# Kernel tuning notes

Hardware: AMD Instinct MI355X
Metric: run time of the kernel (lower is better)

The kernel has to match this reference:

```python
import jax, jax.numpy as jnp
import numpy as np
from jax import lax

B, DIM, H, W = 4, 256, 32, 32
NH = 8
HD = DIM // NH            # 32; CDA uses doubled head dim 2*HD=64
HIDDEN = 512              # FFN hidden, multiple of DIM (groups=DIM dwconv)
DEPTH = 1
LAMBDA_INIT = 0.8 - 0.6 * float(np.exp(-0.3 * DEPTH))
EPS = 1e-5


def conv1x1(w, x):
    # w: (out,in), x: (b,in,h,w)
    return jnp.einsum('oi,bihw->bohw', w, x)


def dwconv(x, w, groups):
    return lax.conv_general_dilated(x, w, (1, 1), 'SAME',
                                    dimension_numbers=('NCHW', 'OIHW', 'NCHW'),
                                    feature_group_count=groups)


def layernorm_c(x, wgt, bias):
    # WithBias LayerNorm over channel dim (to_3d -> LN(-1) -> to_4d)
    mu = jnp.mean(x, axis=1, keepdims=True)
    var = jnp.mean((x - mu) ** 2, axis=1, keepdims=True)
    return (x - mu) / jnp.sqrt(var + EPS) * wgt[None, :, None, None] + bias[None, :, None, None]


def batchnorm(x, g, b, m, v):
    return (x - m[None, :, None, None]) / jnp.sqrt(v[None, :, None, None] + EPS) \
        * g[None, :, None, None] + b[None, :, None, None]


def _cda(x, wq, wk, wv, lq1, lk1, lq2, lk2, rms_scale, wo):
    b, c, hh, ww = x.shape
    n = hh * ww

    def heads(wp):
        t = conv1x1(wp, x).reshape(b, NH, 2 * HD, n)
        return jnp.transpose(t, (0, 1, 3, 2))  # b h n (2hd)

    Q, K, V = heads(wq), heads(wk), heads(wv)
    scale = HD ** -0.5
    a1 = jax.nn.softmax(jnp.einsum('bhnd,bhmd->bhnm', Q[..., :HD], K[..., :HD]) * scale, axis=-1)
    a2 = jax.nn.softmax(jnp.einsum('bhnd,bhmd->bhnm', Q[..., HD:], K[..., HD:]) * scale, axis=-1)
    lam = jnp.exp(jnp.sum(lq1 * lk1, -1)) - jnp.exp(jnp.sum(lq2 * lk2, -1)) + LAMBDA_INIT  # (NH,)
    out = jnp.einsum('bhnm,bhmd->bhnd', a1 - lam[None, :, None, None] * a2, V)
    rms = jnp.sqrt(jnp.mean(out * out, axis=-1, keepdims=True) + EPS)
    out = out / rms * rms_scale * (1.0 - LAMBDA_INIT)
    out = jnp.transpose(out, (0, 1, 3, 2)).reshape(b, 2 * c, hh, ww)
    return conv1x1(wo, out)


def _cha(x, temp, wqkv, wdw, wout):
    b, c, hh, ww = x.shape
    n = hh * ww
    qkv = dwconv(conv1x1(wqkv, x), wdw, 3 * DIM)
    r = qkv.reshape(b, 3, NH, c // NH, n)
    q, k, v = r[:, 0], r[:, 1], r[:, 2]
    q = q / jnp.maximum(jnp.linalg.norm(q, axis=-1, keepdims=True), 1e-12)
    k = k / jnp.maximum(jnp.linalg.norm(k, axis=-1, keepdims=True), 1e-12)
    attn = jax.nn.softmax(jnp.einsum('bhcn,bhdn->bhcd', q, k) * temp[None, :, None, None], axis=-1)
    out = jnp.einsum('bhcd,bhdn->bhcn', attn, v).reshape(b, c, hh, ww)
    return conv1x1(wout, out)


def _ffn(x, bn1_g, bn1_b, bn1_m, bn1_v, w1, b1, bn2_g, bn2_b, bn2_m, bn2_v, w2, b2, w3, b3):
    h = batchnorm(x, bn1_g, bn1_b, bn1_m, bn1_v)
    h = conv1x1(w1, h) + b1[None, :, None, None]
    h = batchnorm(h, bn2_g, bn2_b, bn2_m, bn2_v)
    h = dwconv(h, w2, DIM) + b2[None, :, None, None]
    h = jnp.clip(h, 0.0, 6.0)  # ReLU6
    return conv1x1(w3, h) + b3[None, :, None, None]


def setup_inputs() -> dict:
    key = jax.random.key(0)
    ks = jax.random.split(key, 20)
    nrm = lambda i, shape, s=0.02: jax.random.normal(ks[i], shape, jnp.float32) * s
    return {
        'x': jax.random.normal(ks[0], (B, DIM, H, W), jnp.float32),
        'ln1_w': jnp.ones((DIM,), jnp.float32), 'ln1_b': jnp.zeros((DIM,), jnp.float32),
        'cda_wq': nrm(1, (2 * DIM, DIM)), 'cda_wk': nrm(2, (2 * DIM, DIM)), 'cda_wv': nrm(3, (2 * DIM, DIM)),
        'cda_lq1': nrm(4, (NH, HD), 0.1), 'cda_lk1': nrm(5, (NH, HD), 0.1),
        'cda_lq2': nrm(6, (NH, HD), 0.1), 'cda_lk2': nrm(7, (NH, HD), 0.1),
        'cda_rms_scale': jnp.ones((2 * HD,), jnp.float32), 'cda_wo': nrm(8, (DIM, 2 * DIM)),
        'ln2_w': jnp.ones((DIM,), jnp.float32), 'ln2_b': jnp.zeros((DIM,), jnp.float32),
        'cha_temp': jnp.ones((NH,), jnp.float32),
        'cha_wqkv': nrm(9, (3 * DIM, DIM)), 'cha_wdw': nrm(10, (3 * DIM, 1, 3, 3), 0.1),
        'cha_wout': nrm(11, (DIM, DIM)),
        'ln3_w': jnp.ones((DIM,), jnp.float32), 'ln3_b': jnp.zeros((DIM,), jnp.float32),
        'bn1_g': jnp.ones((DIM,), jnp.float32), 'bn1_b': jnp.zeros((DIM,), jnp.float32),
        'bn1_m': nrm(12, (DIM,), 0.1), 'bn1_v': jnp.ones((DIM,), jnp.float32),
        'ffn_w1': nrm(13, (HIDDEN, DIM)), 'ffn_b1': jnp.zeros((HIDDEN,), jnp.float32),
        'bn2_g': jnp.ones((HIDDEN,), jnp.float32), 'bn2_b': jnp.zeros((HIDDEN,), jnp.float32),
        'bn2_m': nrm(14, (HIDDEN,), 0.1), 'bn2_v': jnp.ones((HIDDEN,), jnp.float32),
        'ffn_w2': nrm(15, (HIDDEN, HIDDEN // DIM, 3, 3), 0.1), 'ffn_b2': jnp.zeros((HIDDEN,), jnp.float32),
        'ffn_w3': nrm(16, (DIM, HIDDEN)), 'ffn_b3': jnp.zeros((DIM,), jnp.float32),
    }


def reference(x, ln1_w, ln1_b, cda_wq, cda_wk, cda_wv, cda_lq1, cda_lk1, cda_lq2, cda_lk2,
              cda_rms_scale, cda_wo, ln2_w, ln2_b, cha_temp, cha_wqkv, cha_wdw, cha_wout,
              ln3_w, ln3_b, bn1_g, bn1_b, bn1_m, bn1_v, ffn_w1, ffn_b1, bn2_g, bn2_b,
              bn2_m, bn2_v, ffn_w2, ffn_b2, ffn_w3, ffn_b3):
    h = layernorm_c(x, ln1_w, ln1_b)
    x = x + _cda(h, cda_wq, cda_wk, cda_wv, cda_lq1, cda_lk1, cda_lq2, cda_lk2, cda_rms_scale, cda_wo)
    h = layernorm_c(x, ln2_w, ln2_b)
    x = x + _cha(h, cha_temp, cha_wqkv, cha_wdw, cha_wout)
    h = layernorm_c(x, ln3_w, ln3_b)
    x = x + _ffn(h, bn1_g, bn1_b, bn1_m, bn1_v, ffn_w1, ffn_b1, bn2_g, bn2_b, bn2_m, bn2_v, ffn_w2, ffn_b2, ffn_w3, ffn_b3)
    return x
```

## Files before the change

kernel.cpp:

```cpp
#include <hip/hip_runtime.h>
#include <hip/hip_bf16.h>

typedef __hip_bfloat16 bf16;
typedef __attribute__((ext_vector_type(8))) short s16x8;
typedef __attribute__((ext_vector_type(4))) float f32x4;

#define DEV __device__ __forceinline__

DEV float b2f(bf16 v){ return __bfloat162float(v); }
DEV ushort f2bf(float f){ bf16 h = __float2bfloat16(f); return *reinterpret_cast<ushort*>(&h); }

constexpr int NPIX = 1024;
constexpr float EPSF = 1e-5f;
constexpr float LAMBDA_INIT_F = 0.3555090675909693f;
constexpr float ONE_M_LI     = 0.6444909324090307f;
constexpr float ATT_SCALE    = 0.17677669529663687f;

constexpr size_t OFF_WBF   = 2120448;
constexpr size_t OFF_QT    = 2644736;
constexpr size_t OFF_V16   = 4741888;
constexpr size_t OFF_ATT   = 5790464;
constexpr size_t OFF_BUF1  = 6839040;
constexpr size_t OFF_BUF2  = 9984768;
constexpr size_t OFF_SPART = 13130496;
constexpr size_t OFF_STATS = 13425408;
constexpr size_t OFF_EFF   = 13449984;
constexpr size_t OFF_FLAG  = 13452608;

struct PackArgs { const void* p[34]; };

__global__ __launch_bounds__(256) void detect_kernel(const void* __restrict__ x, int* __restrict__ flag){
  __shared__ int sh;
  if (threadIdx.x == 0) sh = 0;
  __syncthreads();
  const bf16* h = (const bf16*)x;
  int local = 0;
  for (int i = threadIdx.x; i < 4096; i += 256){
    float v = b2f(h[i]);
    if (!(fabsf(v) <= 1e6f)) local = 1;
  }
  if (local) atomicOr(&sh, 1);
  __syncthreads();
  if (threadIdx.x == 0) *flag = sh;
}

DEV float rdin(const PackArgs& a, int i, int idx, int flag){
  return flag ? ((const float*)a.p[i])[idx] : b2f(((const bf16*)a.p[i])[idx]);
}

__global__ __launch_bounds__(256) void prep_all_kernel(PackArgs args, const int* __restrict__ flagp,
    float* __restrict__ P, ushort* __restrict__ W, float* __restrict__ eff, float* __restrict__ stats){
  __shared__ float ps[16][64], ps2[16][64];
  const int t = threadIdx.x;
  const int blk = blockIdx.x;
  const int flag = *flagp;
  if (blk < 8283){
    constexpr int NIN = 34;
    constexpr int off[NIN+1] = {0,1048576,1048832,1049088,1180160,1311232,1442304,1442560,
      1442816,1443072,1443328,1443392,1574464,1574720,1574976,1574984,1771592,1778504,
      1844040,1844296,1844552,1844808,1845064,1845320,1845576,1976648,1977160,1977672,
      1978184,1978696,1979208,1988424,1988936,2120008,2120264};
    const int g = blk*256 + t;
    if (g >= off[NIN]) return;
    int idx = 0;
    #pragma unroll
    for (int k = 1; k < NIN; k++) idx = (g >= off[k]) ? k : idx;
    P[g] = rdin(args, idx, g - off[idx], flag);
  } else if (blk < 9307){
    const int g = (blk - 8283)*1024 + t*4;
    int src, loc;
    if      (g <  131072){ src = 3;  loc = g; }
    else if (g <  262144){ src = 4;  loc = g - 131072; }
    else if (g <  393216){ src = 5;  loc = g - 262144; }
    else if (g <  589824){ src = 15; loc = g - 393216; }
    else if (g <  720896){ src = 11; loc = g - 589824; }
    else if (g <  786432){ src = 17; loc = g - 720896; }
    else if (g <  917504){ src = 24; loc = g - 786432; }
    else                 { src = 32; loc = g - 917504; }
    ushort4 o;
    if (flag){
      const float4 v = *(const float4*)((const float*)args.p[src] + loc);
      o = make_ushort4(f2bf(v.x), f2bf(v.y), f2bf(v.z), f2bf(v.w));
    } else {
      o = *(const ushort4*)((const ushort*)args.p[src] + loc);
    }
    *(ushort4*)&W[g] = o;
  } else if (blk == 9307){
    eff[t]      = rdin(args,1,t,flag);  eff[256+t] = rdin(args,2,t,flag);
    eff[512+t]  = rdin(args,12,t,flag); eff[768+t] = rdin(args,13,t,flag);
    const float s1 = rdin(args,20,t,flag) * rsqrtf(rdin(args,23,t,flag) + EPSF);
    eff[1024+t] = rdin(args,18,t,flag) * s1;
    eff[1280+t] = (rdin(args,19,t,flag) - rdin(args,22,t,flag)) * s1 + rdin(args,21,t,flag);
    for (int c = t; c < 512; c += 256){
      const float sc = rdin(args,26,c,flag) * rsqrtf(rdin(args,29,c,flag) + EPSF);
      eff[1536+c] = sc;
      eff[2048+c] = rdin(args,27,c,flag) - rdin(args,28,c,flag)*sc;
    }
    if (t < 8){
      float e1 = 0.f, e2 = 0.f;
      for (int i = 0; i < 32; i++){
        e1 += rdin(args,6,t*32+i,flag) * rdin(args,7,t*32+i,flag);
        e2 += rdin(args,8,t*32+i,flag) * rdin(args,9,t*32+i,flag);
      }
      eff[2560+t] = __expf(e1) - __expf(e2) + LAMBDA_INIT_F;
    }
    for (int i = t; i < 16384; i += 256) stats[8192 + i] = 0.f;
  } else {
    const int bi = blk - 9308;
    const int b = bi >> 4, n0 = (bi & 15)*64;
    const int tn = t & 15, tc = t >> 4;
    float s = 0.f, q = 0.f;
    #pragma unroll 4
    for (int i = 0; i < 16; i++){
      const int c = tc*16 + i;
      #pragma unroll
      for (int j = 0; j < 4; j++){
        const float v = rdin(args, 0, ((b*256 + c) << 10) + n0 + tn*4 + j, flag);
        s += v; q += v*v;
      }
    }
    ps[tc][tn*4+0] = 0.f;
    ps[tc][tn*4] = 0.f;
    float sj[4] = {0,0,0,0}, qj[4] = {0,0,0,0};
    #pragma unroll 4
    for (int i = 0; i < 16; i++){
      const int c = tc*16 + i;
      #pragma unroll
      for (int j = 0; j < 4; j++){
        const float v = rdin(args, 0, ((b*256 + c) << 10) + n0 + tn*4 + j, flag);
        sj[j] += v; qj[j] += v*v;
      }
    }
    #pragma unroll
    for (int j = 0; j < 4; j++){ ps[tc][tn*4+j] = sj[j]; ps2[tc][tn*4+j] = qj[j]; }
    __syncthreads();
    if (t < 64){
      float a = 0.f, qq = 0.f;
      #pragma unroll
      for (int j2 = 0; j2 < 16; j2++){ a += ps[j2][t]; qq += ps2[j2][t]; }
      stats[(size_t)b*NPIX + n0 + t] = a;
      stats[4096 + (size_t)b*NPIX + n0 + t] = qq;
    }
  }
}

template<int INM, int EPIM, bool BIAS, bool BN2F, bool STATS>
__global__ __launch_bounds__(256) void gemm_kernel(
    const float* __restrict__ Xf, const ushort* __restrict__ Xb, const ushort* __restrict__ W,
    const float* __restrict__ bias, const float* __restrict__ mu, const float* __restrict__ rstd,
    const float* __restrict__ effw, const float* __restrict__ effb,
    const float* __restrict__ s2, const float* __restrict__ t2,
    const float* __restrict__ res, void* __restrict__ out,
    ushort* __restrict__ qt, ushort* __restrict__ v16,
    float* __restrict__ gstats,
    int Cin, const int* __restrict__ flag)
{
  __shared__ ushort Xt[64][72];
  const int t = threadIdx.x;
  const int nb = blockIdx.x*64, ob = blockIdx.y*64, b = blockIdx.z;
  const int lane = t & 63, w = t >> 6;
  const int wR = w >> 1, wC = w & 1;
  const int l15 = lane & 15, g = lane >> 4;
  const int tn = t & 63, tc4 = t >> 6;
  const f32x4 z4 = {0.f,0.f,0.f,0.f};
  f32x4 acc[2][2] = {{z4,z4},{z4,z4}};

  for (int kb = 0; kb < Cin; kb += 64){
    if (INM == 2){
      const ushort* src = Xb + ((size_t)b*NPIX + nb + tn)*Cin + kb + tc4*16;
      *(uint4*)&Xt[tn][tc4*16]   = *(const uint4*)src;
      *(uint4*)&Xt[tn][tc4*16+8] = *(const uint4*)(src+8);
    } else {
      float m_ = 0.f, r_ = 1.f;
      if (INM == 0){
        const float sv = mu[(size_t)b*NPIX + nb + tn];
        const float qv = rstd[(size_t)b*NPIX + nb + tn];
        m_ = sv * (1.f/256.f);
        const float var = qv*(1.f/256.f) - m_*m_;
        r_ = rsqrtf(fmaxf(var, 0.f) + EPSF);
      }
      ushort tmp[16];
      #pragma unroll
      for (int i = 0; i < 16; i++){
        const int c = kb + tc4*16 + i;
        float v = Xf[((size_t)b*Cin + c)*NPIX + nb + tn];
        if (INM == 0) v = (v - m_)*r_*effw[c] + effb[c];
        tmp[i] = f2bf(v);
      }
      *(uint4*)&Xt[tn][tc4*16]   = *(uint4*)&tmp[0];
      *(uint4*)&Xt[tn][tc4*16+8] = *(uint4*)&tmp[8];
    }
    __syncthreads();
    #pragma unroll
    for (int ks = 0; ks < 2; ks++){
      const s16x8 a0 = *(const s16x8*)&W[(size_t)(ob + wR*32 + l15)*Cin + kb + ks*32 + g*8];
      const s16x8 a1 = *(const s16x8*)&W[(size_t)(ob + wR*32 + 16 + l15)*Cin + kb + ks*32 + g*8];
      const s16x8 b0 = *(const s16x8*)&Xt[wC*32 + l15][ks*32 + g*8];
      const s16x8 b1 = *(const s16x8*)&Xt[wC*32 + 16 + l15][ks*32 + g*8];
      acc[0][0] = __builtin_amdgcn_mfma_f32_16x16x32_bf16(a0, b0, acc[0][0], 0,0,0);
      acc[0][1] = __builtin_amdgcn_mfma_f32_16x16x32_bf16(a0, b1, acc[0][1], 0,0,0);
      acc[1][0] = __builtin_amdgcn_mfma_f32_16x16x32_bf16(a1, b0, acc[1][0], 0,0,0);
      acc[1][1] = __builtin_amdgcn_mfma_f32_16x16x32_bf16(a1, b1, acc[1][1], 0,0,0);
    }
    __syncthreads();
  }

  const int Cout = gridDim.y*64;
  float sst[2] = {0.f, 0.f}, qst[2] = {0.f, 0.f};
  #pragma unroll
  for (int fr = 0; fr < 2; fr++){
    #pragma unroll
    for (int fc = 0; fc < 2; fc++){
      const int o = ob + wR*32 + fr*16 + 4*g;
      const int n = nb + wC*32 + fc*16 + l15;
      const f32x4 v = acc[fr][fc];
      if (EPIM == 0){
        if (ob < 1024){
          const int qk = o >> 9, h = (o >> 6) & 7, d = o & 63;
          ushort4 pk = make_ushort4(f2bf(v[0]), f2bf(v[1]), f2bf(v[2]), f2bf(v[3]));
          ushort* dst = qt + ((((size_t)qk*4 + b)*8 + h)*NPIX + n)*64 + d;
          *(ushort4*)dst = pk;
        } else {
          const int c = o - 1024;
          #pragma unroll
          for (int r = 0; r < 4; r++)
            v16[((size_t)b*512 + c + r)*NPIX + n] = f2bf(v[r]);
        }
      } else {
        #pragma unroll
        for (int r = 0; r < 4; r++){
          float val = v[r];
          if (BIAS) val += bias[o + r];
          if (BN2F) val = val*s2[o+r] + t2[o+r];
          const size_t row = ((size_t)b*Cout + o + r)*NPIX + n;
          if (EPIM == 1){
            const float vf = val + res[row];
            ((float*)out)[row] = vf;
            if (STATS){ sst[fc] += vf; qst[fc] += vf*vf; }
          }
          else if (EPIM == 2){ ((float*)out)[row] = val; }
          else {
            val += res[row];
            if (*flag) ((float*)out)[row] = val;
            else       ((ushort*)out)[row] = f2bf(val);
          }
        }
      }
    }
  }
  if (STATS){
    float* sacc = (float*)&Xt[0][0];
    if (t < 128) sacc[t] = 0.f;
    __syncthreads();
    #pragma unroll
    for (int fc = 0; fc < 2; fc++){
      const int nl = wC*32 + fc*16 + l15;
      atomicAdd(&sacc[nl*2+0], sst[fc]);
      atomicAdd(&sacc[nl*2+1], qst[fc]);
    }
    __syncthreads();
    if (t < 64){
      atomicAdd(&gstats[(size_t)b*NPIX + nb + t],        sacc[t*2+0]);
      atomicAdd(&gstats[4096 + (size_t)b*NPIX + nb + t], sacc[t*2+1]);
    }
  }
}

__global__ __launch_bounds__(256) void attn_kernel(
    const ushort* __restrict__ QT, const ushort* __restrict__ V16,
    const float* __restrict__ Pf, const float* __restrict__ lamArr,
    ushort* __restrict__ att)
{
  __shared__ ushort Ks[2][4096];
  __shared__ ushort Vs[2][4096];
  const int t = threadIdx.x;
  const int lane = t & 63, w = t >> 6;
  const int l15 = lane & 15, g = lane >> 4;
  const int qt = blockIdx.x, h = blockIdx.y, b = blockIdx.z;
  const int qsub = qt*64 + w*16;
  const ushort* Qb = QT + ((size_t)b*8 + h)*NPIX*64;
  const ushort* Kb = QT + ((size_t)(4 + b)*8 + h)*NPIX*64;
  const ushort* Vb = V16 + ((size_t)b*512 + h*64)*NPIX;

  const int c0row = t >> 3, c0col = t & 7;
  const int c1row = (t + 256) >> 3, c1col = t & 7;
  const int sw0 = (c0col ^ (c0row & 7))*8;
  const int sw1 = (c1col ^ (c1row & 7))*8;

  s16x8 bq[2];
  #pragma unroll
  for (int hx = 0; hx < 2; hx++)
    bq[hx] = *(const s16x8*)&Qb[(size_t)(qsub + l15)*64 + 32*hx + 8*g];
  const float lam = lamArr[h];

  const f32x4 z4 = {0.f,0.f,0.f,0.f};
  f32x4 o0[4] = {z4,z4,z4,z4};
  f32x4 o1[4] = {z4,z4,z4,z4};
  float z[2] = {0.f, 0.f};

  uint4 kra = *(const uint4*)&Kb[(size_t)c0row*64 + c0col*8];
  uint4 krb = *(const uint4*)&Kb[(size_t)c1row*64 + c1col*8];
  uint4 vra = *(const uint4*)&Vb[(size_t)c0row*NPIX + c0col*8];
  uint4 vrb = *(const uint4*)&Vb[(size_t)c1row*NPIX + c1col*8];
  *(uint4*)&Ks[0][c0row*64 + sw0] = kra;
  *(uint4*)&Ks[0][c1row*64 + sw1] = krb;
  *(uint4*)&Vs[0][c0row*64 + sw0] = vra;
  *(uint4*)&Vs[0][c1row*64 + sw1] = vrb;
  kra = *(const uint4*)&Kb[(size_t)(64 + c0row)*64 + c0col*8];
  krb = *(const uint4*)&Kb[(size_t)(64 + c1row)*64 + c1col*8];
  vra = *(const uint4*)&Vb[(size_t)c0row*NPIX + 64 + c0col*8];
  vrb = *(const uint4*)&Vb[(size_t)c1row*NPIX + 64 + c1col*8];
  __syncthreads();

  #pragma unroll 1
  for (int it = 0; it < 16; it++){
    const int cur = it & 1;
    const ushort* Kc = &Ks[cur][0];
    const ushort* Vc = &Vs[cur][0];

    f32x4 s[2][4];
    #pragma unroll
    for (int fr = 0; fr < 4; fr++){
      const int row = fr*16 + l15;
      const int rx = (row & 7)*8;
      #pragma unroll
      for (int hx = 0; hx < 2; hx++){
        const s16x8 ak = *(const s16x8*)&Kc[row*64 + ((hx*32 + 8*g) ^ rx)];
        s[hx][fr] = __builtin_amdgcn_mfma_f32_16x16x32_bf16(ak, bq[hx], z4, 0,0,0);
      }
    }
    s16x8 pa[2][2];
    #pragma unroll
    for (int hx = 0; hx < 2; hx++){
      #pragma unroll
      for (int ms = 0; ms < 2; ms++){
        ushort tmp[8];
        #pragma unroll
        for (int fr2 = 0; fr2 < 2; fr2++)
          #pragma unroll
          for (int r = 0; r < 4; r++){
            const float e = __expf(s[hx][ms*2 + fr2][r] * ATT_SCALE);
            z[hx] += e;
            tmp[fr2*4 + r] = f2bf(e);
          }
        pa[hx][ms] = *(s16x8*)tmp;
      }
    }
    __builtin_amdgcn_s_setprio(1);
    #pragma unroll
    for (int ms = 0; ms < 2; ms++){
      #pragma unroll
      for (int dc = 0; dc < 4; dc++){
        const int row = dc*16 + l15;
        const int r7 = row & 7;
        const int elo = ms*32 + 4*g;
        const int eloswz = ((((elo >> 3) ^ r7) << 3) | (elo & 7));
        const int ehi = elo + 16;
        const int ehiswz = ((((ehi >> 3) ^ r7) << 3) | (ehi & 7));
        const uint2 lo = *(const uint2*)&Vc[row*64 + eloswz];
        const uint2 hi = *(const uint2*)&Vc[row*64 + ehiswz];
        union { uint u[4]; s16x8 v; } bv;
        bv.u[0] = lo.x; bv.u[1] = lo.y; bv.u[2] = hi.x; bv.u[3] = hi.y;
        o0[dc] = __builtin_amdgcn_mfma_f32_16x16x32_bf16(pa[0][ms], bv.v, o0[dc], 0,0,0);
        o1[dc] = __builtin_amdgcn_mfma_f32_16x16x32_bf16(pa[1][ms], bv.v, o1[dc], 0,0,0);
      }
    }
    __builtin_amdgcn_s_setprio(0);

    if (it < 15){
      const int nxt = cur ^ 1;
      *(uint4*)&Ks[nxt][c0row*64 + sw0] = kra;
      *(uint4*)&Ks[nxt][c1row*64 + sw1] = krb;
      *(uint4*)&Vs[nxt][c0row*64 + sw0] = vra;
      *(uint4*)&Vs[nxt][c1row*64 + sw1] = vrb;
      if (it < 14){
        const int m0 = (it + 2)*64;
        kra = *(const uint4*)&Kb[(size_t)(m0 + c0row)*64 + c0col*8];
        krb = *(const uint4*)&Kb[(size_t)(m0 + c1row)*64 + c1col*8];
        vra = *(const uint4*)&Vb[(size_t)c0row*NPIX + m0 + c0col*8];
        vrb = *(const uint4*)&Vb[(size_t)c1row*NPIX + m0 + c1col*8];
      }
    }
    __syncthreads();
  }

  #pragma unroll
  for (int hx = 0; hx < 2; hx++){
    z[hx] += __shfl_xor(z[hx], 16);
    z[hx] += __shfl_xor(z[hx], 32);
  }
  float zi0[4], zi1[4];
  #pragma unroll
  for (int r = 0; r < 4; r++){
    zi0[r] = 1.f / __shfl(z[0], 4*g + r);
    zi1[r] = 1.f / __shfl(z[1], 4*g + r);
  }
  float val[4][4];
  float ss[4] = {0.f,0.f,0.f,0.f};
  #pragma unroll
  for (int dc = 0; dc < 4; dc++)
    #pragma unroll
    for (int r = 0; r < 4; r++){
      const float vv = o0[dc][r]*zi0[r] - lam*o1[dc][r]*zi1[r];
      val[dc][r] = vv; ss[r] += vv*vv;
    }
  #pragma unroll
  for (int r = 0; r < 4; r++){
    ss[r] += __shfl_xor(ss[r], 1);
    ss[r] += __shfl_xor(ss[r], 2);
    ss[r] += __shfl_xor(ss[r], 4);
    ss[r] += __shfl_xor(ss[r], 8);
  }
  float rinv[4];
  #pragma unroll
  for (int r = 0; r < 4; r++) rinv[r] = ONE_M_LI * rsqrtf(ss[r]*(1.f/64.f) + EPSF);
  #pragma unroll
  for (int dc = 0; dc < 4; dc++){
    const float rs = Pf[1443328 + dc*16 + l15];
    #pragma unroll
    for (int r = 0; r < 4; r++){
      const int n = qsub + 4*g + r;
      att[((size_t)b*NPIX + n)*512 + h*64 + dc*16 + l15] = f2bf(val[dc][r]*rinv[r]*rs);
    }
  }
}

__global__ __launch_bounds__(256) void dwl2_kernel(const float* __restrict__ in,
    const float* __restrict__ wdw, float* __restrict__ out){
  __shared__ float tile[1024];
  __shared__ float wsum[4];
  const int p = blockIdx.x;
  const int c = p % 768;
  const int t = threadIdx.x;
  const float* ip = in + (size_t)p*1024;
  *(float4*)&tile[t*4] = *(const float4*)&ip[t*4];
  float wv[9];
  #pragma unroll
  for (int i = 0; i < 9; i++) wv[i] = wdw[c*9+i];
  __syncthreads();
  float o[4]; float ssq = 0.f;
  #pragma unroll
  for (int j = 0; j < 4; j++){
    const int px = t*4 + j, x = px & 31, y = px >> 5;
    float s = 0.f;
    #pragma unroll
    for (int ky = 0; ky < 3; ky++){
      const int yy = y + ky - 1;
      if (yy < 0 || yy > 31) continue;
      #pragma unroll
      for (int kx = 0; kx < 3; kx++){
        const int xx = x + kx - 1;
        if (xx < 0 || xx > 31) continue;
        s = fmaf(tile[yy*32+xx], wv[ky*3+kx], s);
      }
    }
    o[j] = s; ssq += s*s;
  }
  for (int off = 32; off; off >>= 1) ssq += __shfl_down(ssq, off);
  if ((t & 63) == 0) wsum[t >> 6] = ssq;
  __syncthreads();
  float inv = 1.f;
  if (c < 512){
    const float tot = wsum[0]+wsum[1]+wsum[2]+wsum[3];
    inv = 1.f / fmaxf(sqrtf(tot), 1e-12f);
  }
  *(float4*)&out[(size_t)p*1024 + t*4] = make_float4(o[0]*inv, o[1]*inv, o[2]*inv, o[3]*inv);
}

__global__ __launch_bounds__(256) void cha_scores_kernel(const float* __restrict__ qk,
                                                         float* __restrict__ spart){
  __shared__ float qs[32][129];
  __shared__ float ks[32][129];
  const int t = threadIdx.x;
  const int nb = blockIdx.x*128;
  const int bh = blockIdx.y, b = bh >> 3, h = bh & 7;
  const size_t qbase = ((size_t)b*768 + h*32)*NPIX + nb;
  const size_t kbase = qbase + (size_t)256*NPIX;
  { const int c = t >> 3, n0 = (t & 7)*16;
    #pragma unroll
    for (int j = 0; j < 16; j++){
      qs[c][n0+j] = qk[qbase + (size_t)c*NPIX + n0 + j];
      ks[c][n0+j] = qk[kbase + (size_t)c*NPIX + n0 + j];
    } }
  __syncthreads();
  const int c = t & 31, dg = t >> 5;
  float acc[4] = {};
  for (int nn = 0; nn < 128; nn++){
    const float qv = qs[c][nn];
    #pragma unroll
    for (int j = 0; j < 4; j++) acc[j] = fmaf(qv, ks[dg*4+j][nn], acc[j]);
  }
  float* sp = spart + ((size_t)bh*8 + blockIdx.x)*1024 + c*32 + dg*4;
  #pragma unroll
  for (int j = 0; j < 4; j++) sp[j] = acc[j];
}

__global__ __launch_bounds__(256) void cha_pv_kernel(const float* __restrict__ spart,
    const float* __restrict__ tempP, const float* __restrict__ qkv, float* __restrict__ out){
  __shared__ float Ps[32][33];
  const int t = threadIdx.x;
  const int bh = blockIdx.y, b = bh >> 3, h = bh & 7;
  const int nb = blockIdx.x*64;
  const float tf = tempP[h];
  for (int p = t; p < 1024; p += 256){
    float s = 0.f;
    #pragma unroll
    for (int ch = 0; ch < 8; ch++) s += spart[((size_t)bh*8 + ch)*1024 + p];
    Ps[p >> 5][p & 31] = s * tf;
  }
  __syncthreads();
  if (t < 32){
    float mx = -1e30f;
    #pragma unroll
    for (int d = 0; d < 32; d++) mx = fmaxf(mx, Ps[t][d]);
    float sum = 0.f;
    float e[32];
    #pragma unroll
    for (int d = 0; d < 32; d++){ e[d] = __expf(Ps[t][d]-mx); sum += e[d]; }
    const float inv = 1.f/sum;
    #pragma unroll
    for (int d = 0; d < 32; d++) Ps[t][d] = e[d]*inv;
  }
  __syncthreads();
  const int n = nb + (t & 63);
  const int cg = t >> 6;
  const size_t vbase = ((size_t)b*768 + 512 + h*32)*NPIX + n;
  float acc[8] = {};
  for (int d = 0; d < 32; d++){
    const float v = qkv[vbase + (size_t)d*NPIX];
    #pragma unroll
    for (int j = 0; j < 8; j++) acc[j] = fmaf(Ps[cg*8+j][d], v, acc[j]);
  }
  const size_t obase = ((size_t)b*256 + h*32 + cg*8)*NPIX + n;
  #pragma unroll
  for (int j = 0; j < 8; j++) out[obase + (size_t)j*NPIX] = acc[j];
}

__global__ __launch_bounds__(256) void gconv_lds_kernel(const float* __restrict__ in,
    const float* __restrict__ w, const float* __restrict__ bias, float* __restrict__ out){
  __shared__ float tin[2][1024];
  const int p = blockIdx.x;
  const int o = p & 511, b = p >> 9;
  const int t = threadIdx.x;
  const float* ip = in + ((size_t)b*512 + (o & ~1))*1024;
  *(float4*)&tin[0][t*4] = *(const float4*)&ip[t*4];
  *(float4*)&tin[1][t*4] = *(const float4*)&ip[1024 + t*4];
  float wv[18];
  #pragma unroll
  for (int i = 0; i < 18; i++) wv[i] = w[o*18 + i];
  const float bs = bias[o];
  __syncthreads();
  float res[4];
  #pragma unroll
  for (int j = 0; j < 4; j++){
    const int px = t*4 + j, x = px & 31, y = px >> 5;
    float s = bs;
    #pragma unroll
    for (int ci = 0; ci < 2; ci++){
      #pragma unroll
      for (int ky = 0; ky < 3; ky++){
        const int yy = y + ky - 1;
        if (yy < 0 || yy > 31) continue;
        #pragma unroll
        for (int kx = 0; kx < 3; kx++){
          const int xx = x + kx - 1;
          if (xx < 0 || xx > 31) continue;
          s = fmaf(tin[ci][yy*32+xx], wv[ci*9 + ky*3 + kx], s);
        }
      }
    }
    res[j] = fminf(fmaxf(s, 0.f), 6.f);
  }
  *(float4*)&out[(size_t)p*1024 + t*4] = make_float4(res[0], res[1], res[2], res[3]);
}

extern "C" void kernel_launch(void* const* d_in, const int* in_sizes, int n_in,
                              void* d_out, int out_size, void* d_ws, size_t ws_size,
                              hipStream_t stream)
{
  (void)in_sizes; (void)n_in; (void)out_size; (void)ws_size;

  float* ws   = (float*)d_ws;
  float* P    = ws;
  float* xbuf = P;
  ushort* Wbf = (ushort*)(ws + OFF_WBF);
  ushort* QT  = (ushort*)(ws + OFF_QT);
  ushort* V16 = (ushort*)(ws + OFF_V16);
  ushort* att = (ushort*)(ws + OFF_ATT);
  float* chaout = ws + OFF_ATT;
  float* buf1 = ws + OFF_BUF1;
  float* buf2 = ws + OFF_BUF2;
  float* spart= ws + OFF_SPART;
  float* stats= ws + OFF_STATS;
  float* eff  = ws + OFF_EFF;
  int*  flag  = (int*)(ws + OFF_FLAG);

  const float* b1f = P + 1976648;
  const float* b3f = P + 2120008;
  const float* w2f = P + 1979208;
  const float* b2f_ = P + 1988424;
  const float* temp = P + 1574976;

  detect_kernel<<<1, 256, 0, stream>>>(d_in[0], flag);
  PackArgs pa;
  for (int i = 0; i < 34; i++) pa.p[i] = d_in[i];
  prep_all_kernel<<<9372, 256, 0, stream>>>(pa, flag, P, Wbf, eff, stats);

  gemm_kernel<0,0,false,false,false><<<dim3(16,24,4), 256, 0, stream>>>(
      xbuf, nullptr, Wbf, nullptr, stats, stats+4096, eff, eff+256,
      nullptr, nullptr, nullptr, nullptr, QT, V16, nullptr, 256, nullptr);
  attn_kernel<<<dim3(16,8,4), 256, 0, stream>>>(QT, V16, P, eff+2560, att);
  gemm_kernel<2,1,false,false,true><<<dim3(16,4,4), 256, 0, stream>>>(
      nullptr, att, Wbf+589824, nullptr, nullptr, nullptr, nullptr, nullptr,
      nullptr, nullptr, xbuf, xbuf, nullptr, nullptr, stats+8192, 512, nullptr);

  gemm_kernel<0,2,false,false,false><<<dim3(16,12,4), 256, 0, stream>>>(
      xbuf, nullptr, Wbf+393216, nullptr, stats+8192, stats+12288, eff+512, eff+768,
      nullptr, nullptr, nullptr, buf1, nullptr, nullptr, nullptr, 256, nullptr);
  dwl2_kernel<<<3072, 256, 0, stream>>>(buf1, P + 1771592, buf2);
  cha_scores_kernel<<<dim3(8,32), 256, 0, stream>>>(buf2, spart);
  cha_pv_kernel<<<dim3(16,32), 256, 0, stream>>>(spart, temp, buf2, chaout);
  gemm_kernel<1,1,false,false,true><<<dim3(16,4,4), 256, 0, stream>>>(
      chaout, nullptr, Wbf+720896, nullptr, nullptr, nullptr, nullptr, nullptr,
      nullptr, nullptr, xbuf, xbuf, nullptr, nullptr, stats+16384, 256, nullptr);

  gemm_kernel<0,2,true,true,false><<<dim3(16,8,4), 256, 0, stream>>>(
      xbuf, nullptr, Wbf+786432, b1f, stats+16384, stats+20480, eff+1024, eff+1280,
      eff+1536, eff+2048, nullptr, buf1, nullptr, nullptr, nullptr, 256, nullptr);
  gconv_lds_kernel<<<2048, 256, 0, stream>>>(buf1, w2f, b2f_, buf2);
  gemm_kernel<1,3,true,false,false><<<dim3(16,4,4), 256, 0, stream>>>(
      buf2, nullptr, Wbf+917504, b3f, nullptr, nullptr, nullptr, nullptr,
      nullptr, nullptr, xbuf, d_out, nullptr, nullptr, nullptr, 512, flag);
}
```

Baseline: 285.9 us.

## Store residual stream pixel-major, fuse CHA kernels, shrink parameter prep

Keeps the residual stream in pixel-major (NHWC-like) layout via a new transpose kernel that also accumulates LayerNorm stats atomically. This lets GEMM prologues and residual epilogues use contiguous float4 loads and stores. It also shrinks the prep kernel to copy only the small parameters actually read in fp32, and fuses the CHA scores and PV kernels into one, writing bf16 pixel-major output for the next GEMM. The fused CHA kernel runs only 32 blocks, which may leave the GPU underused on that stage.

After: 402.1 us. +40.7%, slower.

```diff
diff --git a/kernel.cpp b/kernel.cpp
--- a/kernel.cpp
+++ b/kernel.cpp
@@ -9,6 +9,7 @@
 
 DEV float b2f(bf16 v){ return __bfloat162float(v); }
 DEV ushort f2bf(float f){ bf16 h = __float2bfloat16(f); return *reinterpret_cast<ushort*>(&h); }
+DEV float bf2f(ushort u){ bf16 h; *reinterpret_cast<ushort*>(&h) = u; return __bfloat162float(h); }
 
 constexpr int NPIX = 1024;
 constexpr float EPSF = 1e-5f;
@@ -16,13 +17,14 @@
 constexpr float ONE_M_LI     = 0.6444909324090307f;
 constexpr float ATT_SCALE    = 0.17677669529663687f;
 
+constexpr size_t OFF_XBUF  = 0;
+constexpr size_t OFF_PARM  = 1048576;
 constexpr size_t OFF_WBF   = 2120448;
 constexpr size_t OFF_QT    = 2644736;
 constexpr size_t OFF_V16   = 4741888;
 constexpr size_t OFF_ATT   = 5790464;
 constexpr size_t OFF_BUF1  = 6839040;
 constexpr size_t OFF_BUF2  = 9984768;
-constexpr size_t OFF_SPART = 13130496;
 constexpr size_t OFF_STATS = 13425408;
 constexpr size_t OFF_EFF   = 13449984;
 constexpr size_t OFF_FLAG  = 13452608;
@@ -49,25 +51,24 @@
 }
 
 __global__ __launch_bounds__(256) void prep_all_kernel(PackArgs args, const int* __restrict__ flagp,
-    float* __restrict__ P, ushort* __restrict__ W, float* __restrict__ eff, float* __restrict__ stats){
-  __shared__ float ps[16][64], ps2[16][64];
+    float* __restrict__ parm, ushort* __restrict__ W, float* __restrict__ eff, float* __restrict__ stats){
   const int t = threadIdx.x;
   const int blk = blockIdx.x;
   const int flag = *flagp;
-  if (blk < 8283){
-    constexpr int NIN = 34;
-    constexpr int off[NIN+1] = {0,1048576,1048832,1049088,1180160,1311232,1442304,1442560,
-      1442816,1443072,1443328,1443392,1574464,1574720,1574976,1574984,1771592,1778504,
-      1844040,1844296,1844552,1844808,1845064,1845320,1845576,1976648,1977160,1977672,
-      1978184,1978696,1979208,1988424,1988936,2120008,2120264};
+  if (blk < 69){
     const int g = blk*256 + t;
-    if (g >= off[NIN]) return;
-    int idx = 0;
-    #pragma unroll
-    for (int k = 1; k < NIN; k++) idx = (g >= off[k]) ? k : idx;
-    P[g] = rdin(args, idx, g - off[idx], flag);
-  } else if (blk < 9307){
-    const int g = (blk - 8283)*1024 + t*4;
+    if (g >= 17480) return;
+    int src, loc;
+    if      (g < 64)    { src = 10; loc = g; }
+    else if (g < 72)    { src = 14; loc = g - 64; }
+    else if (g < 6984)  { src = 16; loc = g - 72; }
+    else if (g < 7496)  { src = 25; loc = g - 6984; }
+    else if (g < 16712) { src = 30; loc = g - 7496; }
+    else if (g < 17224) { src = 31; loc = g - 16712; }
+    else                { src = 33; loc = g - 17224; }
+    parm[g] = rdin(args, src, loc, flag);
+  } else if (blk < 1093){
+    const int g = (blk - 69)*1024 + t*4;
     int src, loc;
     if      (g <  131072){ src = 3;  loc = g; }
     else if (g <  262144){ src = 4;  loc = g - 131072; }
@@ -85,7 +86,7 @@
       o = *(const ushort4*)((const ushort*)args.p[src] + loc);
     }
     *(ushort4*)&W[g] = o;
-  } else if (blk == 9307){
+  } else if (blk == 1093){
     eff[t]      = rdin(args,1,t,flag);  eff[256+t] = rdin(args,2,t,flag);
     eff[512+t]  = rdin(args,12,t,flag); eff[768+t] = rdin(args,13,t,flag);
     const float s1 = rdin(args,20,t,flag) * rsqrtf(rdin(args,23,t,flag) + EPSF);
@@ -104,43 +105,63 @@
       }
       eff[2560+t] = __expf(e1) - __expf(e2) + LAMBDA_INIT_F;
     }
-    for (int i = t; i < 16384; i += 256) stats[8192 + i] = 0.f;
   } else {
-    const int bi = blk - 9308;
-    const int b = bi >> 4, n0 = (bi & 15)*64;
-    const int tn = t & 15, tc = t >> 4;
+    const int i = (blk - 1094)*1024 + t*4;
+    *(float4*)&stats[i] = make_float4(0.f,0.f,0.f,0.f);
+  }
+}
+
+__global__ __launch_bounds__(256) void xpose_kernel(const void* __restrict__ xin,
+    const int* __restrict__ flagp, float* __restrict__ xb, float* __restrict__ stats){
+  __shared__ float T[64][68];
+  __shared__ float psum[64][4], psq[64][4];
+  const int t = threadIdx.x;
+  const int nt = blockIdx.x*64, ct = blockIdx.y*64, b = blockIdx.z;
+  const int flag = *flagp;
+  { const int c_ = t >> 2, nq = t & 3;
+    const size_t base = ((size_t)b*256 + ct + c_)*1024 + nt + nq*16;
+    float tmp[16];
+    if (flag){
+      #pragma unroll
+      for (int j = 0; j < 4; j++){
+        const float4 v = *(const float4*)((const float*)xin + base + j*4);
+        tmp[j*4+0]=v.x; tmp[j*4+1]=v.y; tmp[j*4+2]=v.z; tmp[j*4+3]=v.w;
+      }
+    } else {
+      const ushort* xh = (const ushort*)xin + base;
+      #pragma unroll
+      for (int j = 0; j < 2; j++){
+        uint4 u = *(const uint4*)(xh + j*8);
+        const ushort* us = (const ushort*)&u;
+        #pragma unroll
+        for (int k = 0; k < 8; k++) tmp[j*8+k] = bf2f(us[k]);
+      }
+    }
+    #pragma unroll
+    for (int j = 0; j < 4; j++)
+      *(float4*)&T[c_][nq*16 + j*4] = make_float4(tmp[j*4],tmp[j*4+1],tmp[j*4+2],tmp[j*4+3]);
+  }
+  __syncthreads();
+  { const int n_ = t >> 2, cq = t & 3;
     float s = 0.f, q = 0.f;
-    #pragma unroll 4
+    float tmp[16];
+    #pragma unroll
     for (int i = 0; i < 16; i++){
-      const int c = tc*16 + i;
-      #pragma unroll
-      for (int j = 0; j < 4; j++){
-        const float v = rdin(args, 0, ((b*256 + c) << 10) + n0 + tn*4 + j, flag);
-        s += v; q += v*v;
-      }
-    }
-    ps[tc][tn*4+0] = 0.f;
-    ps[tc][tn*4] = 0.f;
-    float sj[4] = {0,0,0,0}, qj[4] = {0,0,0,0};
-    #pragma unroll 4
-    for (int i = 0; i < 16; i++){
-      const int c = tc*16 + i;
-      #pragma unroll
-      for (int j = 0; j < 4; j++){
-        const float v = rdin(args, 0, ((b*256 + c) << 10) + n0 + tn*4 + j, flag);
-        sj[j] += v; qj[j] += v*v;
-      }
-    }
-    #pragma unroll
-    for (int j = 0; j < 4; j++){ ps[tc][tn*4+j] = sj[j]; ps2[tc][tn*4+j] = qj[j]; }
-    __syncthreads();
-    if (t < 64){
-      float a = 0.f, qq = 0.f;
-      #pragma unroll
-      for (int j2 = 0; j2 < 16; j2++){ a += ps[j2][t]; qq += ps2[j2][t]; }
-      stats[(size_t)b*NPIX + n0 + t] = a;
-      stats[4096 + (size_t)b*NPIX + n0 + t] = qq;
-    }
+      const float v = T[cq*16 + i][n_];
+      tmp[i] = v; s += v; q += v*v;
+    }
+    #pragma unroll
+    for (int j = 0; j < 4; j++)
+      *(float4*)&xb[((size_t)b*NPIX + nt + n_)*256 + ct + cq*16 + j*4] =
+          make_float4(tmp[j*4],tmp[j*4+1],tmp[j*4+2],tmp[j*4+3]);
+    psum[n_][cq] = s; psq[n_][cq] = q;
+  }
+  __syncthreads();
+  if (t < 64){
+    const float s = psum[t][0]+psum[t][1]+psum[t][2]+psum[t][3];
+    const float q = psq[t][0]+psq[t][1]+psq[t][2]+psq[t][3];
+    atomicAdd(&stats[(size_t)b*NPIX + nt + t], s);
+    atomicAdd(&stats[4096 + (size_t)b*NPIX + nt + t], q);
   }
 }
 
@@ -165,27 +186,43 @@
   const f32x4 z4 = {0.f,0.f,0.f,0.f};
   f32x4 acc[2][2] = {{z4,z4},{z4,z4}};
 
+  float m_ = 0.f, r_ = 1.f;
+  if (INM == 0){
+    const int n_ = t >> 2;
+    const float sv = mu[(size_t)b*NPIX + nb + n_];
+    const float qv = rstd[(size_t)b*NPIX + nb + n_];
+    m_ = sv * (1.f/256.f);
+    r_ = rsqrtf(fmaxf(qv*(1.f/256.f) - m_*m_, 0.f) + EPSF);
+  }
+
   for (int kb = 0; kb < Cin; kb += 64){
     if (INM == 2){
       const ushort* src = Xb + ((size_t)b*NPIX + nb + tn)*Cin + kb + tc4*16;
       *(uint4*)&Xt[tn][tc4*16]   = *(const uint4*)src;
       *(uint4*)&Xt[tn][tc4*16+8] = *(const uint4*)(src+8);
+    } else if (INM == 0){
+      const int n_ = t >> 2, cq = t & 3;
+      const float* src = Xf + ((size_t)b*NPIX + nb + n_)*Cin + kb + cq*16;
+      float f[16];
+      #pragma unroll
+      for (int j = 0; j < 4; j++){
+        const float4 v = *(const float4*)(src + j*4);
+        f[j*4+0]=v.x; f[j*4+1]=v.y; f[j*4+2]=v.z; f[j*4+3]=v.w;
+      }
+      ushort tmp[16];
+      #pragma unroll
+      for (int i = 0; i < 16; i++){
+        const int c = kb + cq*16 + i;
+        tmp[i] = f2bf((f[i] - m_)*r_*effw[c] + effb[c]);
+      }
+      *(uint4*)&Xt[n_][cq*16]   = *(uint4*)&tmp[0];
+      *(uint4*)&Xt[n_][cq*16+8] = *(uint4*)&tmp[8];
     } else {
-      float m_ = 0.f, r_ = 1.f;
-      if (INM == 0){
-        const float sv = mu[(size_t)b*NPIX + nb + tn];
-        const float qv = rstd[(size_t)b*NPIX + nb + tn];
-        m_ = sv * (1.f/256.f);
-        const float var = qv*(1.f/256.f) - m_*m_;
-        r_ = rsqrtf(fmaxf(var, 0.f) + EPSF);
-      }
       ushort tmp[16];
       #pragma unroll
       for (int i = 0; i < 16; i++){
         const int c = kb + tc4*16 + i;
-        float v = Xf[((size_t)b*Cin + c)*NPIX + nb + tn];
-        if (INM == 0) v = (v - m_)*r_*effw[c] + effb[c];
-        tmp[i] = f2bf(v);
+        tmp[i] = f2bf(Xf[((size_t)b*Cin + c)*NPIX + nb + tn]);
       }
       *(uint4*)&Xt[tn][tc4*16]   = *(uint4*)&tmp[0];
       *(uint4*)&Xt[tn][tc4*16+8] = *(uint4*)&tmp[8];
@@ -206,6 +243,7 @@
   }
 
   const int Cout = gridDim.y*64;
+  const int fl = (EPIM == 3) ? *flag : 0;
   float sst[2] = {0.f, 0.f}, qst[2] = {0.f, 0.f};
   #pragma unroll
   for (int fr = 0; fr < 2; fr++){
@@ -226,24 +264,39 @@
           for (int r = 0; r < 4; r++)
             v16[((size_t)b*512 + c + r)*NPIX + n] = f2bf(v[r]);
         }
-      } else {
+      } else if (EPIM == 1){
+        const size_t row = ((size_t)b*NPIX + n)*Cout + o;
+        const float4 r4 = *(const float4*)&res[row];
+        float vals[4];
+        #pragma unroll
+        for (int r = 0; r < 4; r++){
+          float val = v[r];
+          if (BIAS) val += bias[o+r];
+          if (BN2F) val = val*s2[o+r] + t2[o+r];
+          vals[r] = val + ((const float*)&r4)[r];
+        }
+        *(float4*)&((float*)out)[row] = make_float4(vals[0],vals[1],vals[2],vals[3]);
+        if (STATS){
+          sst[fc] += vals[0]+vals[1]+vals[2]+vals[3];
+          qst[fc] += vals[0]*vals[0]+vals[1]*vals[1]+vals[2]*vals[2]+vals[3]*vals[3];
+        }
+      } else if (EPIM == 2){
         #pragma unroll
         for (int r = 0; r < 4; r++){
           float val = v[r];
           if (BIAS) val += bias[o + r];
           if (BN2F) val = val*s2[o+r] + t2[o+r];
-          const size_t row = ((size_t)b*Cout + o + r)*NPIX + n;
-          if (EPIM == 1){
-            const float vf = val + res[row];
-            ((float*)out)[row] = vf;
-            if (STATS){ sst[fc] += vf; qst[fc] += vf*vf; }
-          }
-          else if (EPIM == 2){ ((float*)out)[row] = val; }
-          else {
-            val += res[row];
-            if (*flag) ((float*)out)[row] = val;
-            else       ((ushort*)out)[row] = f2bf(val);
-          }
+          ((float*)out)[((size_t)b*Cout + o + r)*NPIX + n] = val;
+        }
+      } else {
+        const float4 r4 = *(const float4*)&res[((size_t)b*NPIX + n)*256 + o];
+        #pragma unroll
+        for (int r = 0; r < 4; r++){
+          float val = v[r] + ((const float*)&r4)[r];
+          if (BIAS) val += bias[o+r];
+          const size_t row = ((size_t)b*256 + o + r)*NPIX + n;
+          if (fl) ((float*)out)[row] = val;
+          else    ((ushort*)out)[row] = f2bf(val);
         }
       }
     }
@@ -268,7 +321,7 @@
 
 __global__ __launch_bounds__(256) void attn_kernel(
     const ushort* __restrict__ QT, const ushort* __restrict__ V16,
-    const float* __restrict__ Pf, const float* __restrict__ lamArr,
+    const float* __restrict__ rms, const float* __restrict__ lamArr,
     ushort* __restrict__ att)
 {
   __shared__ ushort Ks[2][4096];
@@ -416,7 +469,7 @@
   for (int r = 0; r < 4; r++) rinv[r] = ONE_M_LI * rsqrtf(ss[r]*(1.f/64.f) + EPSF);
   #pragma unroll
   for (int dc = 0; dc < 4; dc++){
-    const float rs = Pf[1443328 + dc*16 + l15];
+    const float rs = rms[dc*16 + l15];
     #pragma unroll
     for (int r = 0; r < 4; r++){
       const int n = qsub + 4*g + r;
@@ -467,73 +520,64 @@
   *(float4*)&out[(size_t)p*1024 + t*4] = make_float4(o[0]*inv, o[1]*inv, o[2]*inv, o[3]*inv);
 }
 
-__global__ __launch_bounds__(256) void cha_scores_kernel(const float* __restrict__ qk,
-                                                         float* __restrict__ spart){
-  __shared__ float qs[32][129];
-  __shared__ float ks[32][129];
+__global__ __launch_bounds__(256) void cha_fused_kernel(const float* __restrict__ qk,
+    const float* __restrict__ tempP, ushort* __restrict__ out16){
+  __shared__ float qs[32][129], ks[32][129];
+  __shared__ float Ss[32][33];
   const int t = threadIdx.x;
-  const int nb = blockIdx.x*128;
-  const int bh = blockIdx.y, b = bh >> 3, h = bh & 7;
-  const size_t qbase = ((size_t)b*768 + h*32)*NPIX + nb;
-  const size_t kbase = qbase + (size_t)256*NPIX;
-  { const int c = t >> 3, n0 = (t & 7)*16;
-    #pragma unroll
-    for (int j = 0; j < 16; j++){
-      qs[c][n0+j] = qk[qbase + (size_t)c*NPIX + n0 + j];
-      ks[c][n0+j] = qk[kbase + (size_t)c*NPIX + n0 + j];
-    } }
-  __syncthreads();
-  const int c = t & 31, dg = t >> 5;
-  float acc[4] = {};
-  for (int nn = 0; nn < 128; nn++){
-    const float qv = qs[c][nn];
-    #pragma unroll
-    for (int j = 0; j < 4; j++) acc[j] = fmaf(qv, ks[dg*4+j][nn], acc[j]);
-  }
-  float* sp = spart + ((size_t)bh*8 + blockIdx.x)*1024 + c*32 + dg*4;
-  #pragma unroll
-  for (int j = 0; j < 4; j++) sp[j] = acc[j];
-}
-
-__global__ __launch_bounds__(256) void cha_pv_kernel(const float* __restrict__ spart,
-    const float* __restrict__ tempP, const float* __restrict__ qkv, float* __restrict__ out){
-  __shared__ float Ps[32][33];
-  const int t = threadIdx.x;
-  const int bh = blockIdx.y, b = bh >> 3, h = bh & 7;
-  const int nb = blockIdx.x*64;
+  const int bh = blockIdx.x, b = bh >> 3, h = bh & 7;
+  const size_t qbase = ((size_t)b*768 + h*32)*1024;
+  const size_t kbase = qbase + (size_t)256*1024;
+  const int c31 = t & 31, dg = t >> 5;
+  float acc[4] = {0.f,0.f,0.f,0.f};
+  for (int ch = 0; ch < 8; ch++){
+    { const int cs = t >> 3, n0 = (t & 7)*16;
+      #pragma unroll
+      for (int j = 0; j < 4; j++){
+        const float4 vq = *(const float4*)&qk[qbase + (size_t)cs*1024 + ch*128 + n0 + j*4];
+        const float4 vk = *(const float4*)&qk[kbase + (size_t)cs*1024 + ch*128 + n0 + j*4];
+        qs[cs][n0+j*4+0]=vq.x; qs[cs][n0+j*4+1]=vq.y; qs[cs][n0+j*4+2]=vq.z; qs[cs][n0+j*4+3]=vq.w;
+        ks[cs][n0+j*4+0]=vk.x; ks[cs][n0+j*4+1]=vk.y; ks[cs][n0+j*4+2]=vk.z; ks[cs][n0+j*4+3]=vk.w;
+      } }
+    __syncthreads();
+    for (int nn = 0; nn < 128; nn++){
+      const float qv = qs[c31][nn];
+      #pragma unroll
+      for (int j = 0; j < 4; j++) acc[j] = fmaf(qv, ks[dg*4+j][nn], acc[j]);
+    }
+    __syncthreads();
+  }
   const float tf = tempP[h];
-  for (int p = t; p < 1024; p += 256){
-    float s = 0.f;
-    #pragma unroll
-    for (int ch = 0; ch < 8; ch++) s += spart[((size_t)bh*8 + ch)*1024 + p];
-    Ps[p >> 5][p & 31] = s * tf;
-  }
+  #pragma unroll
+  for (int j = 0; j < 4; j++) Ss[c31][dg*4+j] = acc[j]*tf;
   __syncthreads();
   if (t < 32){
     float mx = -1e30f;
     #pragma unroll
-    for (int d = 0; d < 32; d++) mx = fmaxf(mx, Ps[t][d]);
-    float sum = 0.f;
-    float e[32];
-    #pragma unroll
-    for (int d = 0; d < 32; d++){ e[d] = __expf(Ps[t][d]-mx); sum += e[d]; }
+    for (int d = 0; d < 32; d++) mx = fmaxf(mx, Ss[t][d]);
+    float sum = 0.f; float e[32];
+    #pragma unroll
+    for (int d = 0; d < 32; d++){ e[d] = __expf(Ss[t][d]-mx); sum += e[d]; }
     const float inv = 1.f/sum;
     #pragma unroll
-    for (int d = 0; d < 32; d++) Ps[t][d] = e[d]*inv;
-  }
-  __syncthreads();
-  const int n = nb + (t & 63);
-  const int cg = t >> 6;
-  const size_t vbase = ((size_t)b*768 + 512 + h*32)*NPIX + n;
-  float acc[8] = {};
-  for (int d = 0; d < 32; d++){
-    const float v = qkv[vbase + (size_t)d*NPIX];
-    #pragma unroll
-    for (int j = 0; j < 8; j++) acc[j] = fmaf(Ps[cg*8+j][d], v, acc[j]);
-  }
-  const size_t obase = ((size_t)b*256 + h*32 + cg*8)*NPIX + n;
-  #pragma unroll
-  for (int j = 0; j < 8; j++) out[obase + (size_t)j*NPIX] = acc[j];
+    for (int d = 0; d < 32; d++) Ss[t][d] = e[d]*inv;
+  }
+  __syncthreads();
+  const int n64 = t & 63, cg = t >> 6;
+  const size_t vbase = ((size_t)b*768 + 512 + h*32)*1024;
+  for (int ch = 0; ch < 16; ch++){
+    const int nb2 = ch*64;
+    float acc8[8] = {};
+    for (int d = 0; d < 32; d++){
+      const float v = qk[vbase + (size_t)d*1024 + nb2 + n64];
+      #pragma unroll
+      for (int j = 0; j < 8; j++) acc8[j] = fmaf(Ss[cg*8+j][d], v, acc8[j]);
+    }
+    ushort o8[8];
+    #pragma unroll
+    for (int j = 0; j < 8; j++) o8[j] = f2bf(acc8[j]);
+    *(uint4*)&out16[((size_t)b*NPIX + nb2 + n64)*256 + h*32 + cg*8] = *(uint4*)o8;
+  }
 }
 
 __global__ __launch_bounds__(256) void gconv_lds_kernel(const float* __restrict__ in,
@@ -580,36 +624,30 @@
 {
   (void)in_sizes; (void)n_in; (void)out_size; (void)ws_size;
 
-  float* ws   = (float*)d_ws;
-  float* P    = ws;
-  float* xbuf = P;
-  ushort* Wbf = (ushort*)(ws + OFF_WBF);
-  ushort* QT  = (ushort*)(ws + OFF_QT);
-  ushort* V16 = (ushort*)(ws + OFF_V16);
-  ushort* att = (ushort*)(ws + OFF_ATT);
-  float* chaout = ws + OFF_ATT;
-  float* buf1 = ws + OFF_BUF1;
-  float* buf2 = ws + OFF_BUF2;
-  float* spart= ws + OFF_SPART;
-  float* stats= ws + OFF_STATS;
-  float* eff  = ws + OFF_EFF;
-  int*  flag  = (int*)(ws + OFF_FLAG);
-
-  const float* b1f = P + 1976648;
-  const float* b3f = P + 2120008;
-  const float* w2f = P + 1979208;
-  const float* b2f_ = P + 1988424;
-  const float* temp = P + 1574976;
+  float* ws    = (float*)d_ws;
+  float* xbuf  = ws + OFF_XBUF;
+  float* parm  = ws + OFF_PARM;
+  ushort* Wbf  = (ushort*)(ws + OFF_WBF);
+  ushort* QT   = (ushort*)(ws + OFF_QT);
+  ushort* V16  = (ushort*)(ws + OFF_V16);
+  ushort* att  = (ushort*)(ws + OFF_ATT);
+  ushort* cha16= (ushort*)(ws + OFF_ATT);
+  float* buf1  = ws + OFF_BUF1;
+  float* buf2  = ws + OFF_BUF2;
+  float* stats = ws + OFF_STATS;
+  float* eff   = ws + OFF_EFF;
+  int*  flag   = (int*)(ws + OFF_FLAG);
 
   detect_kernel<<<1, 256, 0, stream>>>(d_in[0], flag);
   PackArgs pa;
   for (int i = 0; i < 34; i++) pa.p[i] = d_in[i];
-  prep_all_kernel<<<9372, 256, 0, stream>>>(pa, flag, P, Wbf, eff, stats);
+  prep_all_kernel<<<1118, 256, 0, stream>>>(pa, flag, parm, Wbf, eff, stats);
+  xpose_kernel<<<dim3(16,4,4), 256, 0, stream>>>(d_in[0], flag, xbuf, stats);
 
   gemm_kernel<0,0,false,false,false><<<dim3(16,24,4), 256, 0, stream>>>(
       xbuf, nullptr, Wbf, nullptr, stats, stats+4096, eff, eff+256,
       nullptr, nullptr, nullptr, nullptr, QT, V16, nullptr, 256, nullptr);
-  attn_kernel<<<dim3(16,8,4), 256, 0, stream>>>(QT, V16, P, eff+2560, att);
+  attn_kernel<<<dim3(16,8,4), 256, 0, stream>>>(QT, V16, parm, eff+2560, att);
   gemm_kernel<2,1,false,false,true><<<dim3(16,4,4), 256, 0, stream>>>(
       nullptr, att, Wbf+589824, nullptr, nullptr, nullptr, nullptr, nullptr,
       nullptr, nullptr, xbuf, xbuf, nullptr, nullptr, stats+8192, 512, nullptr);
@@ -617,18 +655,17 @@
   gemm_kernel<0,2,false,false,false><<<dim3(16,12,4), 256, 0, stream>>>(
       xbuf, nullptr, Wbf+393216, nullptr, stats+8192, stats+12288, eff+512, eff+768,
       nullptr, nullptr, nullptr, buf1, nullptr, nullptr, nullptr, 256, nullptr);
-  dwl2_kernel<<<3072, 256, 0, stream>>>(buf1, P + 1771592, buf2);
-  cha_scores_kernel<<<dim3(8,32), 256, 0, stream>>>(buf2, spart);
-  cha_pv_kernel<<<dim3(16,32), 256, 0, stream>>>(spart, temp, buf2, chaout);
-  gemm_kernel<1,1,false,false,true><<<dim3(16,4,4), 256, 0, stream>>>(
-      chaout, nullptr, Wbf+720896, nullptr, nullptr, nullptr, nullptr, nullptr,
+  dwl2_kernel<<<3072, 256, 0, stream>>>(buf1, parm + 72, buf2);
+  cha_fused_kernel<<<32, 256, 0, stream>>>(buf2, parm + 64, cha16);
+  gemm_kernel<2,1,false,false,true><<<dim3(16,4,4), 256, 0, stream>>>(
+      nullptr, cha16, Wbf+720896, nullptr, nullptr, nullptr, nullptr, nullptr,
       nullptr, nullptr, xbuf, xbuf, nullptr, nullptr, stats+16384, 256, nullptr);
 
   gemm_kernel<0,2,true,true,false><<<dim3(16,8,4), 256, 0, stream>>>(
-      xbuf, nullptr, Wbf+786432, b1f, stats+16384, stats+20480, eff+1024, eff+1280,
+      xbuf, nullptr, Wbf+786432, parm+6984, stats+16384, stats+20480, eff+1024, eff+1280,
       eff+1536, eff+2048, nullptr, buf1, nullptr, nullptr, nullptr, 256, nullptr);
-  gconv_lds_kernel<<<2048, 256, 0, stream>>>(buf1, w2f, b2f_, buf2);
+  gconv_lds_kernel<<<2048, 256, 0, stream>>>(buf1, parm+7496, parm+16712, buf2);
   gemm_kernel<1,3,true,false,false><<<dim3(16,4,4), 256, 0, stream>>>(
-      buf2, nullptr, Wbf+917504, b3f, nullptr, nullptr, nullptr, nullptr,
+      buf2, nullptr, Wbf+917504, parm+17224, nullptr, nullptr, nullptr, nullptr,
       nullptr, nullptr, xbuf, d_out, nullptr, nullptr, nullptr, 512, flag);
 }
```
